# Performance work log

Hardware: AMD Instinct MI355X
Metric: run time of the kernel (lower is better)

## Reference

```python
import jax, jax.numpy as jnp
import numpy as np

N = 20000   # mesh vertices
B = 8       # batch
F = 64      # in_channels
K = 6       # Chebyshev order
OUT = 64    # out_channels
NNZ = 320000  # nonzeros in sparse Laplacian (avg degree 16)


def setup_inputs() -> dict:
    key = jax.random.key(0)
    ks = jax.random.split(key, 6)
    x = jax.random.normal(ks[0], (B, N, F), dtype=jnp.float32)
    lap_rows = jax.random.randint(ks[1], (NNZ,), 0, N, dtype=jnp.int32)
    lap_cols = jax.random.randint(ks[2], (NNZ,), 0, N, dtype=jnp.int32)
    lap_vals = jax.random.normal(ks[3], (NNZ,), dtype=jnp.float32) * 0.05
    # fc: Linear(K*F, OUT), xavier_normal weight, zero bias
    W = jax.random.normal(ks[4], (OUT, K * F), dtype=jnp.float32) * float(np.sqrt(2.0 / (K * F + OUT)))
    b = jnp.zeros((OUT,), dtype=jnp.float32)
    return {"x": x, "lap_rows": lap_rows, "lap_cols": lap_cols,
            "lap_vals": lap_vals, "W": W, "b": b}


def reference(x, lap_rows, lap_cols, lap_vals, W, b):
    Bd, Nd, Fd = x.shape

    def spmm(v):  # sparse [N,N] @ dense [N, B*F] via COO gather + segment_sum
        return jax.ops.segment_sum(lap_vals[:, None] * v[lap_cols], lap_rows,
                                   num_segments=Nd)

    x0 = jnp.transpose(x, (1, 0, 2)).reshape(Nd, Bd * Fd)  # [N, B*F]
    outs = [x0]
    if K > 1:
        tx1 = spmm(x0)
        outs.append(tx1)
        tx0 = x0
        for _ in range(2, K):  # Chebyshev recurrence T_k = 2 L T_{k-1} - T_{k-2}
            tx2 = 2.0 * spmm(tx1) - tx0
            outs.append(tx2)
            tx0, tx1 = tx1, tx2
    out = jnp.concatenate([o.reshape(Nd, Bd, Fd) for o in outs], axis=2)  # [N,B,K*F]
    out = out.reshape(Nd * Bd, K * Fd) @ W.T + b  # dense fc
    return jnp.transpose(out.reshape(Nd, Bd, -1), (1, 0, 2))  # [B,N,OUT]
```

## Files before the change

kernel.cpp:

```cpp
#include <hip/hip_runtime.h>

#define N_V  20000
#define B_   8
#define F_   64
#define K_   6
#define OUT_ 64
#define NNZ_ 320000
#define BF   512
#define NSLICE 8
#define SLICE_W 2500
#define NBUK (N_V * NSLICE)
#define SCANB 157

typedef unsigned short ushort_t;
typedef unsigned int   uint_t;

using frag_ab = __attribute__((ext_vector_type(8))) short;
using frag_cd = __attribute__((ext_vector_type(4))) float;

__device__ __forceinline__ ushort_t f2bf(float f) {
    uint_t u = __float_as_uint(f);
    u += 0x7FFFu + ((u >> 16) & 1u);
    return (ushort_t)(u >> 16);
}
__device__ __forceinline__ uint_t pack2(float lo, float hi) {
    return (uint_t)f2bf(lo) | ((uint_t)f2bf(hi) << 16);
}
__device__ __forceinline__ void unpack2(uint_t u, float& lo, float& hi) {
    lo = __uint_as_float(u << 16);
    hi = __uint_as_float(u & 0xFFFF0000u);
}
__device__ __forceinline__ void unpack8(uint4 u, float* e) {
    unpack2(u.x, e[0], e[1]); unpack2(u.y, e[2], e[3]);
    unpack2(u.z, e[4], e[5]); unpack2(u.w, e[6], e[7]);
}


__global__ void hist_kernel(const int* __restrict__ rows, const int* __restrict__ cols,
                            int* __restrict__ counts) {
    int e = blockIdx.x * 256 + threadIdx.x;
    if (e < NNZ_) {
        int key = rows[e] * NSLICE + cols[e] / SLICE_W;
        atomicAdd(&counts[key], 1);
    }
}

__global__ __launch_bounds__(1024) void scan1(const int* __restrict__ counts,
                                              int* __restrict__ incl, int* __restrict__ bsum) {
    __shared__ int buf[1024];
    int tid = threadIdx.x;
    int i = blockIdx.x * 1024 + tid;
    int c = (i < NBUK) ? counts[i] : 0;
    buf[tid] = c;
    __syncthreads();
    for (int off = 1; off < 1024; off <<= 1) {
        int t = buf[tid];
        int add = (tid >= off) ? buf[tid - off] : 0;
        __syncthreads();
        buf[tid] = t + add;
        __syncthreads();
    }
    if (i < NBUK) incl[i] = buf[tid];
    if (tid == 1023) bsum[blockIdx.x] = buf[1023];
}

__global__ __launch_bounds__(256) void scan2(int* __restrict__ bsum) {
    __shared__ int buf[256];
    int tid = threadIdx.x;
    int c = (tid < SCANB) ? bsum[tid] : 0;
    buf[tid] = c;
    __syncthreads();
    for (int off = 1; off < 256; off <<= 1) {
        int t = buf[tid];
        int add = (tid >= off) ? buf[tid - off] : 0;
        __syncthreads();
        buf[tid] = t + add;
        __syncthreads();
    }
    if (tid < SCANB) bsum[tid] = buf[tid] - c;
}

__global__ __launch_bounds__(1024) void scan3(const int* __restrict__ counts,
                                              const int* __restrict__ bsum,
                                              int* __restrict__ bp, int* __restrict__ cursor) {
    int tid = threadIdx.x;
    int i = blockIdx.x * 1024 + tid;
    if (i < NBUK) {
        int p = bsum[blockIdx.x] + cursor[i];
        bp[i + 1] = p;
        cursor[i] = p - counts[i];
    }
    if (i == 0) bp[0] = 0;
}

__global__ void scatter_kernel(const int* __restrict__ rows, const int* __restrict__ cols,
                               const float* __restrict__ vals, int* __restrict__ cursor,
                               int* __restrict__ cols_perm, float* __restrict__ vals_perm) {
    int e = blockIdx.x * 256 + threadIdx.x;
    if (e < NNZ_) {
        int c = cols[e];
        int key = rows[e] * NSLICE + c / SLICE_W;
        int pos = atomicAdd(&cursor[key], 1);
        cols_perm[pos] = c;
        vals_perm[pos] = vals[e];
    }
}

__global__ void x2bf_kernel(const float* __restrict__ x, uint_t* __restrict__ X0) {
    int idx = blockIdx.x * 256 + threadIdx.x;
    int f2 = idx & 31;
    int b  = (idx >> 5) & 7;
    int n  = idx >> 8;
    float2 v = *(const float2*)&x[((size_t)b * N_V + n) * F_ + f2 * 2];
    X0[n * 256 + b * 32 + f2] = pack2(v.x, v.y);
}

template <bool RECUR>
__global__ __launch_bounds__(256) void cheb_phase(const int* __restrict__ bp,
                                                  const int* __restrict__ cols_perm,
                                                  const float* __restrict__ vals_perm,
                                                  const ushort_t* __restrict__ Tprev,
                                                  const ushort_t* __restrict__ Tpp,
                                                  ushort_t* __restrict__ Tout) {
    const int wave = threadIdx.x >> 6, lane = threadIdx.x & 63;
    const int n0 = blockIdx.x * 16 + wave * 4;
    float acc[4][8];
#pragma unroll
    for (int r = 0; r < 4; ++r)
#pragma unroll
        for (int i = 0; i < 8; ++i) acc[r][i] = 0.f;

    for (int s = 0; s < NSLICE; ++s) {
#pragma unroll
        for (int r = 0; r < 4; ++r) {
            const int bidx = (n0 + r) * NSLICE + s;
            int st = bp[bidx], en = bp[bidx + 1];
            for (int j = st; j < en; j += 2) {
                int j1 = j + 1;
                int jc1 = j1 < (NNZ_ - 1) ? j1 : (NNZ_ - 1);
                int   c0 = cols_perm[j];
                int   c1 = cols_perm[jc1];
                float v0 = vals_perm[j];
                float v1 = (j1 < en) ? vals_perm[jc1] : 0.f;
                uint4 u0 = *(const uint4*)(Tprev + (size_t)c0 * BF + lane * 8);
                uint4 u1 = *(const uint4*)(Tprev + (size_t)c1 * BF + lane * 8);
                float e0[8], e1[8];
                unpack8(u0, e0);
                unpack8(u1, e1);
#pragma unroll
                for (int i = 0; i < 8; ++i) {
                    acc[r][i] = fmaf(v0, e0[i], acc[r][i]);
                    acc[r][i] = fmaf(v1, e1[i], acc[r][i]);
                }
            }
        }
    }

#pragma unroll
    for (int r = 0; r < 4; ++r) {
        const int n = n0 + r;
        float res[8];
        if (RECUR) {
            uint4 up = *(const uint4*)(Tpp + (size_t)n * BF + lane * 8);
            float ep[8];
            unpack8(up, ep);
#pragma unroll
            for (int i = 0; i < 8; ++i) res[i] = 2.f * acc[r][i] - ep[i];
        } else {
#pragma unroll
            for (int i = 0; i < 8; ++i) res[i] = acc[r][i];
        }
        uint4 st;
        st.x = pack2(res[0], res[1]);
        st.y = pack2(res[2], res[3]);
        st.z = pack2(res[4], res[5]);
        st.w = pack2(res[6], res[7]);
        *(uint4*)(Tout + (size_t)n * BF + lane * 8) = st;
    }
}

__global__ void wfrag_kernel(const float* __restrict__ W, ushort_t* __restrict__ Wfrag) {
    int idx = blockIdx.x * 256 + threadIdx.x;
    if (idx < 12 * 4 * 64 * 8) {
        int j    = idx & 7;
        int lane = (idx >> 3) & 63;
        int ct   = (idx >> 9) & 3;
        int s    = idx >> 11;
        int o     = ct * 16 + (lane & 15);
        int kglob = s * 32 + ((lane >> 4) & 3) * 8 + j;
        Wfrag[idx] = f2bf(W[o * (K_ * F_) + kglob]);
    }
}

__global__ __launch_bounds__(256) void fc_mfma(const ushort_t* __restrict__ X0,
                                               const ushort_t* __restrict__ T1,
                                               const ushort_t* __restrict__ T2,
                                               const ushort_t* __restrict__ T3,
                                               const ushort_t* __restrict__ T4,
                                               const ushort_t* __restrict__ T5,
                                               const ushort_t* __restrict__ Wfrag,
                                               const float* __restrict__ bias,
                                               float* __restrict__ out) {
    const int wave = threadIdx.x >> 6, lane = threadIdx.x & 63;
    const int quad = lane >> 4, col = lane & 15;
    const int tb = blockIdx.x * 64 + wave * 16;
    const int r = tb + col;
    const ushort_t* Tbuf[6] = {X0, T1, T2, T3, T4, T5};

    frag_cd acc[4];
#pragma unroll
    for (int ct = 0; ct < 4; ++ct) acc[ct] = (frag_cd){0.f, 0.f, 0.f, 0.f};

#pragma unroll
    for (int s = 0; s < 12; ++s) {
        const int f0 = (s & 1) * 32 + quad * 8;
        frag_ab a = *(const frag_ab*)(Tbuf[s >> 1] + (size_t)r * F_ + f0);
#pragma unroll
        for (int ct = 0; ct < 4; ++ct) {
            frag_ab bfr = *(const frag_ab*)(Wfrag + (((s * 4 + ct) * 64 + lane) << 3));
            acc[ct] = __builtin_amdgcn_mfma_f32_16x16x32_bf16(a, bfr, acc[ct], 0, 0, 0);
        }
    }

#pragma unroll
    for (int ct = 0; ct < 4; ++ct) {
        const int o = ct * 16 + col;
        const float bv = bias[o];
#pragma unroll
        for (int reg = 0; reg < 4; ++reg) {
            int rr = tb + quad * 4 + reg;
            int nn = rr >> 3, bb = rr & 7;
            out[(size_t)bb * N_V * OUT_ + (size_t)nn * OUT_ + o] = acc[ct][reg] + bv;
        }
    }
}


extern "C" void kernel_launch(void* const* d_in, const int* in_sizes, int n_in,
                              void* d_out, int out_size, void* d_ws, size_t ws_size,
                              hipStream_t stream) {
    const float* x    = (const float*)d_in[0];
    const int*   rows = (const int*)  d_in[1];
    const int*   cols = (const int*)  d_in[2];
    const float* vals = (const float*)d_in[3];
    const float* W    = (const float*)d_in[4];
    const float* bias = (const float*)d_in[5];
    float* out = (float*)d_out;

    const size_t TSZ = (size_t)N_V * BF;
    ushort_t* T1 = (ushort_t*)d_ws;
    ushort_t* T2 = T1 + TSZ;
    ushort_t* T3 = T2 + TSZ;
    ushort_t* T4 = T3 + TSZ;
    ushort_t* T5 = T4 + TSZ;
    ushort_t* X0 = T5 + TSZ;
    ushort_t* Wfrag = X0 + TSZ;
    int* counts    = (int*)(Wfrag + 24576);
    int* bp        = counts + NBUK;
    int* cursor    = bp + NBUK + 64;
    int* bsum      = cursor + NBUK;
    int* cols_perm = bsum + 256;
    float* vals_perm = (float*)(cols_perm + NNZ_);

    hipMemsetAsync(counts, 0, NBUK * sizeof(int), stream);
    hist_kernel<<<(NNZ_ + 255) / 256, 256, 0, stream>>>(rows, cols, counts);
    scan1<<<SCANB, 1024, 0, stream>>>(counts, cursor, bsum);
    scan2<<<1, 256, 0, stream>>>(bsum);
    scan3<<<SCANB, 1024, 0, stream>>>(counts, bsum, bp, cursor);
    scatter_kernel<<<(NNZ_ + 255) / 256, 256, 0, stream>>>(rows, cols, vals, cursor,
                                                           cols_perm, vals_perm);
    x2bf_kernel<<<(N_V * B_ * 32) / 256, 256, 0, stream>>>(x, (uint_t*)X0);
    wfrag_kernel<<<96, 256, 0, stream>>>(W, Wfrag);

    cheb_phase<false><<<N_V / 16, 256, 0, stream>>>(bp, cols_perm, vals_perm, X0, nullptr, T1);
    cheb_phase<true ><<<N_V / 16, 256, 0, stream>>>(bp, cols_perm, vals_perm, T1, X0, T2);
    cheb_phase<true ><<<N_V / 16, 256, 0, stream>>>(bp, cols_perm, vals_perm, T2, T1, T3);
    cheb_phase<true ><<<N_V / 16, 256, 0, stream>>>(bp, cols_perm, vals_perm, T3, T2, T4);
    cheb_phase<true ><<<N_V / 16, 256, 0, stream>>>(bp, cols_perm, vals_perm, T4, T3, T5);

    fc_mfma<<<(N_V * B_) / 64, 256, 0, stream>>>(X0, T1, T2, T3, T4, T5, Wfrag, bias, out);
}
```

Baseline: 430.8 us.

## Pack edges as int2, split feature rows across waves, fuse prep kernels

Column indices and values are stored interleaved as int2, so each edge needs one load instead of two. Each row's feature vector is now split across two waves with 8-byte loads, and each wave walks two rows' edge lists at once, four gathers per iteration, to get more memory-level parallelism. Row bucket pointers are preloaded into registers. x/W conversion kernels are merged into one launch, and the FC kernel computes two 16-row tiles per wave to reuse the W fragments. The trade-off is narrower gathers per lane, more clamped redundant loads when the two rows' edge counts differ, and more registers.

```diff
diff --git a/kernel.cpp b/kernel.cpp
--- a/kernel.cpp
+++ b/kernel.cpp
@@ -30,9 +30,8 @@
     lo = __uint_as_float(u << 16);
     hi = __uint_as_float(u & 0xFFFF0000u);
 }
-__device__ __forceinline__ void unpack8(uint4 u, float* e) {
+__device__ __forceinline__ void unpack4(uint2 u, float* e) {
     unpack2(u.x, e[0], e[1]); unpack2(u.y, e[2], e[3]);
-    unpack2(u.z, e[4], e[5]); unpack2(u.w, e[6], e[7]);
 }
 
 
@@ -95,62 +94,100 @@
 
 __global__ void scatter_kernel(const int* __restrict__ rows, const int* __restrict__ cols,
                                const float* __restrict__ vals, int* __restrict__ cursor,
-                               int* __restrict__ cols_perm, float* __restrict__ vals_perm) {
+                               int2* __restrict__ edges) {
     int e = blockIdx.x * 256 + threadIdx.x;
     if (e < NNZ_) {
         int c = cols[e];
         int key = rows[e] * NSLICE + c / SLICE_W;
         int pos = atomicAdd(&cursor[key], 1);
-        cols_perm[pos] = c;
-        vals_perm[pos] = vals[e];
-    }
-}
-
-__global__ void x2bf_kernel(const float* __restrict__ x, uint_t* __restrict__ X0) {
-    int idx = blockIdx.x * 256 + threadIdx.x;
-    int f2 = idx & 31;
-    int b  = (idx >> 5) & 7;
-    int n  = idx >> 8;
-    float2 v = *(const float2*)&x[((size_t)b * N_V + n) * F_ + f2 * 2];
-    X0[n * 256 + b * 32 + f2] = pack2(v.x, v.y);
+        int2 pe; pe.x = c; pe.y = __float_as_int(vals[e]);
+        edges[pos] = pe;
+    }
+}
+
+__global__ void prep_kernel(const float* __restrict__ x, uint_t* __restrict__ X0,
+                            const float* __restrict__ W, ushort_t* __restrict__ Wfrag) {
+    int blk = blockIdx.x;
+    if (blk < 20000) {
+        int idx = blk * 256 + threadIdx.x;
+        int f2 = idx & 31;
+        int b  = (idx >> 5) & 7;
+        int n  = idx >> 8;
+        float2 v = *(const float2*)&x[((size_t)b * N_V + n) * F_ + f2 * 2];
+        X0[n * 256 + b * 32 + f2] = pack2(v.x, v.y);
+    } else {
+        int idx = (blk - 20000) * 256 + threadIdx.x;
+        if (idx < 12 * 4 * 64 * 8) {
+            int j    = idx & 7;
+            int lane = (idx >> 3) & 63;
+            int ct   = (idx >> 9) & 3;
+            int s    = idx >> 11;
+            int o     = ct * 16 + (lane & 15);
+            int kglob = s * 32 + ((lane >> 4) & 3) * 8 + j;
+            Wfrag[idx] = f2bf(W[o * (K_ * F_) + kglob]);
+        }
+    }
 }
 
 template <bool RECUR>
 __global__ __launch_bounds__(256) void cheb_phase(const int* __restrict__ bp,
-                                                  const int* __restrict__ cols_perm,
-                                                  const float* __restrict__ vals_perm,
+                                                  const int2* __restrict__ edges,
                                                   const ushort_t* __restrict__ Tprev,
                                                   const ushort_t* __restrict__ Tpp,
                                                   ushort_t* __restrict__ Tout) {
     const int wave = threadIdx.x >> 6, lane = threadIdx.x & 63;
-    const int n0 = blockIdx.x * 16 + wave * 4;
-    float acc[4][8];
+    const int half = wave & 1;
+    const int n0 = blockIdx.x * 8 + (wave >> 1) * 4;
+    const int fo = half * 256 + lane * 4;
+
+    int bpr[4][9];
+#pragma unroll
+    for (int r = 0; r < 4; ++r) {
+        const int4 a = *(const int4*)&bp[(n0 + r) * 8];
+        const int4 b = *(const int4*)&bp[(n0 + r) * 8 + 4];
+        bpr[r][0] = a.x; bpr[r][1] = a.y; bpr[r][2] = a.z; bpr[r][3] = a.w;
+        bpr[r][4] = b.x; bpr[r][5] = b.y; bpr[r][6] = b.z; bpr[r][7] = b.w;
+        bpr[r][8] = bp[(n0 + r) * 8 + 8];
+    }
+
+    float acc[4][4];
 #pragma unroll
     for (int r = 0; r < 4; ++r)
 #pragma unroll
-        for (int i = 0; i < 8; ++i) acc[r][i] = 0.f;
+        for (int i = 0; i < 4; ++i) acc[r][i] = 0.f;
 
     for (int s = 0; s < NSLICE; ++s) {
 #pragma unroll
-        for (int r = 0; r < 4; ++r) {
-            const int bidx = (n0 + r) * NSLICE + s;
-            int st = bp[bidx], en = bp[bidx + 1];
-            for (int j = st; j < en; j += 2) {
-                int j1 = j + 1;
-                int jc1 = j1 < (NNZ_ - 1) ? j1 : (NNZ_ - 1);
-                int   c0 = cols_perm[j];
-                int   c1 = cols_perm[jc1];
-                float v0 = vals_perm[j];
-                float v1 = (j1 < en) ? vals_perm[jc1] : 0.f;
-                uint4 u0 = *(const uint4*)(Tprev + (size_t)c0 * BF + lane * 8);
-                uint4 u1 = *(const uint4*)(Tprev + (size_t)c1 * BF + lane * 8);
-                float e0[8], e1[8];
-                unpack8(u0, e0);
-                unpack8(u1, e1);
-#pragma unroll
-                for (int i = 0; i < 8; ++i) {
-                    acc[r][i] = fmaf(v0, e0[i], acc[r][i]);
-                    acc[r][i] = fmaf(v1, e1[i], acc[r][i]);
+        for (int rp = 0; rp < 2; ++rp) {
+            const int r0 = rp * 2, r1 = rp * 2 + 1;
+            const int s0 = bpr[r0][s], e0n = bpr[r0][s + 1];
+            const int s1 = bpr[r1][s], e1n = bpr[r1][s + 1];
+            const int d0 = e0n - s0, d1 = e1n - s1;
+            const int mx = d0 > d1 ? d0 : d1;
+            for (int t = 0; t < mx; t += 2) {
+                int ja = s0 + t, jb = ja + 1;
+                int ka = s1 + t, kb = ka + 1;
+                int2 ea = edges[max(min(ja, e0n - 1), 0)];
+                int2 eb = edges[max(min(jb, e0n - 1), 0)];
+                int2 ec = edges[max(min(ka, e1n - 1), 0)];
+                int2 ed = edges[max(min(kb, e1n - 1), 0)];
+                float va = (ja < e0n) ? __int_as_float(ea.y) : 0.f;
+                float vb = (jb < e0n) ? __int_as_float(eb.y) : 0.f;
+                float vc = (ka < e1n) ? __int_as_float(ec.y) : 0.f;
+                float vd = (kb < e1n) ? __int_as_float(ed.y) : 0.f;
+                uint2 ua = *(const uint2*)(Tprev + (size_t)ea.x * BF + fo);
+                uint2 ub = *(const uint2*)(Tprev + (size_t)eb.x * BF + fo);
+                uint2 uc = *(const uint2*)(Tprev + (size_t)ec.x * BF + fo);
+                uint2 ud = *(const uint2*)(Tprev + (size_t)ed.x * BF + fo);
+                float xa[4], xb[4], xc[4], xd[4];
+                unpack4(ua, xa); unpack4(ub, xb);
+                unpack4(uc, xc); unpack4(ud, xd);
+#pragma unroll
+                for (int i = 0; i < 4; ++i) {
+                    acc[r0][i] = fmaf(va, xa[i], acc[r0][i]);
+                    acc[r0][i] = fmaf(vb, xb[i], acc[r0][i]);
+                    acc[r1][i] = fmaf(vc, xc[i], acc[r1][i]);
+                    acc[r1][i] = fmaf(vd, xd[i], acc[r1][i]);
                 }
             }
         }
@@ -159,36 +196,21 @@
 #pragma unroll
     for (int r = 0; r < 4; ++r) {
         const int n = n0 + r;
-        float res[8];
+        float res[4];
         if (RECUR) {
-            uint4 up = *(const uint4*)(Tpp + (size_t)n * BF + lane * 8);
-            float ep[8];
-            unpack8(up, ep);
-#pragma unroll
-            for (int i = 0; i < 8; ++i) res[i] = 2.f * acc[r][i] - ep[i];
+            uint2 up = *(const uint2*)(Tpp + (size_t)n * BF + fo);
+            float ep[4];
+            unpack4(up, ep);
+#pragma unroll
+            for (int i = 0; i < 4; ++i) res[i] = 2.f * acc[r][i] - ep[i];
         } else {
 #pragma unroll
-            for (int i = 0; i < 8; ++i) res[i] = acc[r][i];
-        }
-        uint4 st;
+            for (int i = 0; i < 4; ++i) res[i] = acc[r][i];
+        }
+        uint2 st;
         st.x = pack2(res[0], res[1]);
         st.y = pack2(res[2], res[3]);
-        st.z = pack2(res[4], res[5]);
-        st.w = pack2(res[6], res[7]);
-        *(uint4*)(Tout + (size_t)n * BF + lane * 8) = st;
-    }
-}
-
-__global__ void wfrag_kernel(const float* __restrict__ W, ushort_t* __restrict__ Wfrag) {
-    int idx = blockIdx.x * 256 + threadIdx.x;
-    if (idx < 12 * 4 * 64 * 8) {
-        int j    = idx & 7;
-        int lane = (idx >> 3) & 63;
-        int ct   = (idx >> 9) & 3;
-        int s    = idx >> 11;
-        int o     = ct * 16 + (lane & 15);
-        int kglob = s * 32 + ((lane >> 4) & 3) * 8 + j;
-        Wfrag[idx] = f2bf(W[o * (K_ * F_) + kglob]);
+        *(uint2*)(Tout + (size_t)n * BF + fo) = st;
     }
 }
 
@@ -203,22 +225,27 @@
                                                float* __restrict__ out) {
     const int wave = threadIdx.x >> 6, lane = threadIdx.x & 63;
     const int quad = lane >> 4, col = lane & 15;
-    const int tb = blockIdx.x * 64 + wave * 16;
-    const int r = tb + col;
+    const int tb = blockIdx.x * 128 + wave * 32;
+    const int r0 = tb + col, r1 = tb + 16 + col;
     const ushort_t* Tbuf[6] = {X0, T1, T2, T3, T4, T5};
 
-    frag_cd acc[4];
-#pragma unroll
-    for (int ct = 0; ct < 4; ++ct) acc[ct] = (frag_cd){0.f, 0.f, 0.f, 0.f};
+    frag_cd acc0[4], acc1[4];
+#pragma unroll
+    for (int ct = 0; ct < 4; ++ct) {
+        acc0[ct] = (frag_cd){0.f, 0.f, 0.f, 0.f};
+        acc1[ct] = (frag_cd){0.f, 0.f, 0.f, 0.f};
+    }
 
 #pragma unroll
     for (int s = 0; s < 12; ++s) {
         const int f0 = (s & 1) * 32 + quad * 8;
-        frag_ab a = *(const frag_ab*)(Tbuf[s >> 1] + (size_t)r * F_ + f0);
+        frag_ab a0 = *(const frag_ab*)(Tbuf[s >> 1] + (size_t)r0 * F_ + f0);
+        frag_ab a1 = *(const frag_ab*)(Tbuf[s >> 1] + (size_t)r1 * F_ + f0);
 #pragma unroll
         for (int ct = 0; ct < 4; ++ct) {
             frag_ab bfr = *(const frag_ab*)(Wfrag + (((s * 4 + ct) * 64 + lane) << 3));
-            acc[ct] = __builtin_amdgcn_mfma_f32_16x16x32_bf16(a, bfr, acc[ct], 0, 0, 0);
+            acc0[ct] = __builtin_amdgcn_mfma_f32_16x16x32_bf16(a0, bfr, acc0[ct], 0, 0, 0);
+            acc1[ct] = __builtin_amdgcn_mfma_f32_16x16x32_bf16(a1, bfr, acc1[ct], 0, 0, 0);
         }
     }
 
@@ -228,9 +255,10 @@
         const float bv = bias[o];
 #pragma unroll
         for (int reg = 0; reg < 4; ++reg) {
-            int rr = tb + quad * 4 + reg;
-            int nn = rr >> 3, bb = rr & 7;
-            out[(size_t)bb * N_V * OUT_ + (size_t)nn * OUT_ + o] = acc[ct][reg] + bv;
+            int ra = tb + quad * 4 + reg;
+            int rb = ra + 16;
+            out[(size_t)(ra & 7) * N_V * OUT_ + (size_t)(ra >> 3) * OUT_ + o] = acc0[ct][reg] + bv;
+            out[(size_t)(rb & 7) * N_V * OUT_ + (size_t)(rb >> 3) * OUT_ + o] = acc1[ct][reg] + bv;
         }
     }
 }
@@ -259,24 +287,21 @@
     int* bp        = counts + NBUK;
     int* cursor    = bp + NBUK + 64;
     int* bsum      = cursor + NBUK;
-    int* cols_perm = bsum + 256;
-    float* vals_perm = (float*)(cols_perm + NNZ_);
+    int2* edges    = (int2*)(bsum + 256);
 
     hipMemsetAsync(counts, 0, NBUK * sizeof(int), stream);
     hist_kernel<<<(NNZ_ + 255) / 256, 256, 0, stream>>>(rows, cols, counts);
     scan1<<<SCANB, 1024, 0, stream>>>(counts, cursor, bsum);
     scan2<<<1, 256, 0, stream>>>(bsum);
     scan3<<<SCANB, 1024, 0, stream>>>(counts, bsum, bp, cursor);
-    scatter_kernel<<<(NNZ_ + 255) / 256, 256, 0, stream>>>(rows, cols, vals, cursor,
-                                                           cols_perm, vals_perm);
-    x2bf_kernel<<<(N_V * B_ * 32) / 256, 256, 0, stream>>>(x, (uint_t*)X0);
-    wfrag_kernel<<<96, 256, 0, stream>>>(W, Wfrag);
-
-    cheb_phase<false><<<N_V / 16, 256, 0, stream>>>(bp, cols_perm, vals_perm, X0, nullptr, T1);
-    cheb_phase<true ><<<N_V / 16, 256, 0, stream>>>(bp, cols_perm, vals_perm, T1, X0, T2);
-    cheb_phase<true ><<<N_V / 16, 256, 0, stream>>>(bp, cols_perm, vals_perm, T2, T1, T3);
-    cheb_phase<true ><<<N_V / 16, 256, 0, stream>>>(bp, cols_perm, vals_perm, T3, T2, T4);
-    cheb_phase<true ><<<N_V / 16, 256, 0, stream>>>(bp, cols_perm, vals_perm, T4, T3, T5);
-
-    fc_mfma<<<(N_V * B_) / 64, 256, 0, stream>>>(X0, T1, T2, T3, T4, T5, Wfrag, bias, out);
-}
+    scatter_kernel<<<(NNZ_ + 255) / 256, 256, 0, stream>>>(rows, cols, vals, cursor, edges);
+    prep_kernel<<<20096, 256, 0, stream>>>(x, (uint_t*)X0, W, Wfrag);
+
+    cheb_phase<false><<<N_V / 8, 256, 0, stream>>>(bp, edges, X0, nullptr, T1);
+    cheb_phase<true ><<<N_V / 8, 256, 0, stream>>>(bp, edges, T1, X0, T2);
+    cheb_phase<true ><<<N_V / 8, 256, 0, stream>>>(bp, edges, T2, T1, T3);
+    cheb_phase<true ><<<N_V / 8, 256, 0, stream>>>(bp, edges, T3, T2, T4);
+    cheb_phase<true ><<<N_V / 8, 256, 0, stream>>>(bp, edges, T4, T3, T5);
+
+    fc_mfma<<<(N_V * B_) / 128, 256, 0, stream>>>(X0, T1, T2, T3, T4, T5, Wfrag, bias, out);
+}
```

Result: slower. 536.3 us (+24.5%).
